# Kernel optimization log

Hardware: AMD Instinct MI355X
Metric: run time of the kernel (lower is better)

Reference implementation:

```python
import jax, jax.numpy as jnp
import numpy as np

ITERS = 10
EPS = 1e-6
TEMPERATURE = 1.0


def setup_inputs() -> dict:
    key = jax.random.key(0)
    S, E = 524288, 64
    logits = jax.random.normal(key, (S, E), dtype=jnp.float32)
    return {"logits": logits, "top_k": 2}


def reference(logits, top_k):
    s, e = logits.shape
    scores = (logits / TEMPERATURE).astype(jnp.float32)
    scores = scores - jnp.max(scores, axis=-1, keepdims=True)
    q = jnp.exp(scores)
    col_target = float(s) / float(max(e, 1))

    def body(q, _):
        q = q / (jnp.sum(q, axis=1, keepdims=True) + EPS)
        q = q / (jnp.sum(q, axis=0, keepdims=True) + EPS) * col_target
        return q, None

    q, _ = jax.lax.scan(body, q, None, length=ITERS)
    q = q / (jnp.sum(q, axis=1, keepdims=True) + EPS)
    vals, idx = jax.lax.top_k(q, top_k)
    w = vals / (jnp.sum(vals, axis=-1, keepdims=True) + EPS)
    return idx.astype(jnp.int64), w.astype(logits.dtype)
```

## Files before the change

kernel.cpp:

```cpp
#include <hip/hip_runtime.h>
#include <math.h>

#define EPS 1e-6f
#define NE 64
#define THREADS 256
#define WPB 4
#define NBLOCKS 1024
#define NWAVES (NBLOCKS * WPB)
#define ITERS 10
#define PF 4

template <int ctrl>
__device__ __forceinline__ float dppf(float x) {
    return __int_as_float(__builtin_amdgcn_update_dpp(
        0, __float_as_int(x), ctrl, 0xf, 0xf, true));
}
template <int ctrl>
__device__ __forceinline__ int dppi(int x) {
    return __builtin_amdgcn_update_dpp(0, x, ctrl, 0xf, 0xf, true);
}

__device__ __forceinline__ float group16_sum(float v) {
    v += dppf<0xB1>(v);
    v += dppf<0x4E>(v);
    v += dppf<0x141>(v);
    v += dppf<0x140>(v);
    return v;
}

#define ARGMAX_STEP(CTRL)                                      \
    {                                                          \
        float ov = dppf<CTRL>(v);                              \
        int oi = dppi<CTRL>(i);                                \
        if (ov > v || (ov == v && oi < i)) { v = ov; i = oi; } \
    }

__device__ __forceinline__ void group16_argmax(float& v, int& i) {
    ARGMAX_STEP(0xB1)
    ARGMAX_STEP(0x4E)
    ARGMAX_STEP(0x141)
    ARGMAX_STEP(0x140)
}

template <bool FIRST>
__global__ __launch_bounds__(THREADS) void sink_pass(
    const float4* __restrict__ logits4, float* __restrict__ r,
    const float* __restrict__ c, float* __restrict__ Pblk, int nquads) {
    const int lane = threadIdx.x & 63;
    const int wib = threadIdx.x >> 6;
    const int g = lane >> 4;
    const int h = lane & 15;
    const int qpw = nquads / NWAVES;
    const int qbase = (blockIdx.x * WPB + wib) * qpw;

    float4 c4;
    if (FIRST) c4 = make_float4(1.f, 1.f, 1.f, 1.f);
    else       c4 = ((const float4*)c)[h];

    const float4* lp = logits4 + (size_t)qbase * 64 + lane;

    float4 buf[PF];
    float rbuf[PF];
#pragma unroll
    for (int p = 0; p < PF; ++p) buf[p] = lp[(size_t)p * 64];
    if (!FIRST) {
#pragma unroll
        for (int p = 0; p < PF; ++p) rbuf[p] = r[(qbase + p) * 4 + g];
    }

    float4 pacc = {0.f, 0.f, 0.f, 0.f};
    const int nb = qpw / PF;
    for (int b = 0; b < nb; ++b) {
        float4 cur[PF];
        float rcur[PF];
#pragma unroll
        for (int p = 0; p < PF; ++p) {
            cur[p] = buf[p];
            if (!FIRST) rcur[p] = rbuf[p];
        }
        if (b + 1 < nb) {
            const float4* np = lp + (size_t)(b + 1) * PF * 64;
#pragma unroll
            for (int p = 0; p < PF; ++p) buf[p] = np[(size_t)p * 64];
            if (!FIRST) {
#pragma unroll
                for (int p = 0; p < PF; ++p)
                    rbuf[p] = r[(qbase + (b + 1) * PF + p) * 4 + g];
            }
        }
#pragma unroll
        for (int p = 0; p < PF; ++p) {
            float4 q;
            q.x = __expf(cur[p].x); q.y = __expf(cur[p].y);
            q.z = __expf(cur[p].z); q.w = __expf(cur[p].w);
            float s = q.x * c4.x + q.y * c4.y + q.z * c4.z + q.w * c4.w;
            s = group16_sum(s);
            float rold = FIRST ? 1.0f : rcur[p];
            float rnew = rold / (rold * s + EPS);
            int row = (qbase + b * PF + p) * 4 + g;
            if (h == 0) r[row] = rnew;
            pacc.x += q.x * rnew; pacc.y += q.y * rnew;
            pacc.z += q.z * rnew; pacc.w += q.w * rnew;
        }
    }

    __shared__ float4 plds[WPB][64];
    plds[wib][lane] = pacc;
    __syncthreads();
    if (threadIdx.x < NE) {
        int j = threadIdx.x;
        int hh = j >> 2, kk = j & 3;
        float t = 0.f;
#pragma unroll
        for (int w = 0; w < WPB; ++w)
#pragma unroll
            for (int gg = 0; gg < 4; ++gg)
                t += ((const float*)&plds[w][gg * 16 + hh])[kk];
        Pblk[blockIdx.x * NE + j] = t;
    }
}

template <bool FIRST>
__global__ __launch_bounds__(1024) void sink_reduce(
    const float* __restrict__ Pblk, float* __restrict__ c, float col_target) {
    const int j = threadIdx.x & 63;
    const int chunk = threadIdx.x >> 6;
    const int per = NBLOCKS / 16;
    float t = 0.f;
    int b0 = chunk * per;
    for (int b = b0; b < b0 + per; ++b) t += Pblk[b * NE + j];
    __shared__ float lds[16][NE];
    lds[chunk][j] = t;
    __syncthreads();
    if (threadIdx.x < NE) {
        float P = 0.f;
#pragma unroll
        for (int k = 0; k < 16; ++k) P += lds[k][threadIdx.x];
        float cj = FIRST ? 1.0f : c[threadIdx.x];
        c[threadIdx.x] = cj * col_target / (cj * P + EPS);
    }
}

__global__ __launch_bounds__(THREADS) void sink_final(
    const float4* __restrict__ logits4, const float* __restrict__ r,
    const float* __restrict__ c, float2* __restrict__ oidx,
    float2* __restrict__ ow, int nquads) {
    const int lane = threadIdx.x & 63;
    const int wib = threadIdx.x >> 6;
    const int g = lane >> 4;
    const int h = lane & 15;
    const int base_col = h * 4;
    const int qpw = nquads / NWAVES;
    const int qbase = (blockIdx.x * WPB + wib) * qpw;

    const float4 c4 = ((const float4*)c)[h];
    const float4* lp = logits4 + (size_t)qbase * 64 + lane;

    float4 buf[PF];
    float rbuf[PF];
#pragma unroll
    for (int p = 0; p < PF; ++p) buf[p] = lp[(size_t)p * 64];
#pragma unroll
    for (int p = 0; p < PF; ++p) rbuf[p] = r[(qbase + p) * 4 + g];

    const int nb = qpw / PF;
    for (int b = 0; b < nb; ++b) {
        float4 cur[PF];
        float rcur[PF];
#pragma unroll
        for (int p = 0; p < PF; ++p) { cur[p] = buf[p]; rcur[p] = rbuf[p]; }
        if (b + 1 < nb) {
            const float4* np = lp + (size_t)(b + 1) * PF * 64;
#pragma unroll
            for (int p = 0; p < PF; ++p) buf[p] = np[(size_t)p * 64];
#pragma unroll
            for (int p = 0; p < PF; ++p)
                rbuf[p] = r[(qbase + (b + 1) * PF + p) * 4 + g];
        }
#pragma unroll
        for (int p = 0; p < PF; ++p) {
            float4 u;
            u.x = __expf(cur[p].x) * c4.x; u.y = __expf(cur[p].y) * c4.y;
            u.z = __expf(cur[p].z) * c4.z; u.w = __expf(cur[p].w) * c4.w;
            float s = group16_sum(u.x + u.y + u.z + u.w);
            float rold = rcur[p];
            float rnew = rold / (rold * s + EPS);
            float4 val;
            val.x = u.x * rnew; val.y = u.y * rnew;
            val.z = u.z * rnew; val.w = u.w * rnew;

            float v = val.x; int i = base_col;
            if (val.y > v) { v = val.y; i = base_col + 1; }
            if (val.z > v) { v = val.z; i = base_col + 2; }
            if (val.w > v) { v = val.w; i = base_col + 3; }
            group16_argmax(v, i);
            float v1 = v; int i1 = i;

            float4 mv;
            mv.x = (i1 == base_col)     ? -INFINITY : val.x;
            mv.y = (i1 == base_col + 1) ? -INFINITY : val.y;
            mv.z = (i1 == base_col + 2) ? -INFINITY : val.z;
            mv.w = (i1 == base_col + 3) ? -INFINITY : val.w;
            v = mv.x; i = base_col;
            if (mv.y > v) { v = mv.y; i = base_col + 1; }
            if (mv.z > v) { v = mv.z; i = base_col + 2; }
            if (mv.w > v) { v = mv.w; i = base_col + 3; }
            group16_argmax(v, i);
            float v2 = v; int i2 = i;

            if (h == 0) {
                int row = (qbase + b * PF + p) * 4 + g;
                float wsum = v1 + v2 + EPS;
                oidx[row] = make_float2((float)i1, (float)i2);
                ow[row] = make_float2(v1 / wsum, v2 / wsum);
            }
        }
    }
}

extern "C" void kernel_launch(void* const* d_in, const int* in_sizes, int n_in,
                              void* d_out, int out_size, void* d_ws, size_t ws_size,
                              hipStream_t stream) {
    const float* logits = (const float*)d_in[0];
    const int S = in_sizes[0] / NE;
    const int nquads = S / 4;
    const float col_target = (float)S / (float)NE;

    float* r = (float*)d_ws;
    float* c = r + S;
    float* Pblk = c + NE;

    float* out = (float*)d_out;
    float2* oidx = (float2*)out;
    float2* ow = (float2*)(out + (size_t)2 * S);

    const float4* l4 = (const float4*)logits;

    sink_pass<true><<<NBLOCKS, THREADS, 0, stream>>>(l4, r, c, Pblk, nquads);
    sink_reduce<true><<<1, 1024, 0, stream>>>(Pblk, c, col_target);
    for (int it = 1; it < ITERS; ++it) {
        sink_pass<false><<<NBLOCKS, THREADS, 0, stream>>>(l4, r, c, Pblk, nquads);
        sink_reduce<false><<<1, 1024, 0, stream>>>(Pblk, c, col_target);
    }
    sink_final<<<NBLOCKS, THREADS, 0, stream>>>(l4, r, c, oidx, ow, nquads);
}
```

Before: 614.0 us.

## Fuse column reduction into pass kernel via last-block atomic counter

Removes the separate single-block sink_reduce launch after each pass. The last block to finish, found through an atomic counter, now reduces the per-block column partials and updates c. Blocks grow from 256 to 1024 threads and drop from 1024 to 256, which shrinks the partial array. This saves ten launches and their serialization gaps, at the cost of a memset, threadfences, and fewer, larger blocks that may lower occupancy or latency hiding.

```diff
diff --git a/kernel.cpp b/kernel.cpp
--- a/kernel.cpp
+++ b/kernel.cpp
@@ -3,10 +3,10 @@
 
 #define EPS 1e-6f
 #define NE 64
-#define THREADS 256
-#define WPB 4
-#define NBLOCKS 1024
-#define NWAVES (NBLOCKS * WPB)
+#define TPB 1024
+#define WPB 16
+#define NBLK 256
+#define NWAVES (NBLK * WPB)
 #define ITERS 10
 #define PF 4
 
@@ -43,11 +43,13 @@
 }
 
 template <bool FIRST>
-__global__ __launch_bounds__(THREADS) void sink_pass(
+__global__ __launch_bounds__(TPB) void sink_pass(
     const float4* __restrict__ logits4, float* __restrict__ r,
-    const float* __restrict__ c, float* __restrict__ Pblk, int nquads) {
-    const int lane = threadIdx.x & 63;
-    const int wib = threadIdx.x >> 6;
+    float* __restrict__ c, float* __restrict__ Pblk,
+    unsigned* __restrict__ counters, int nquads, float col_target, int it) {
+    const int tid = threadIdx.x;
+    const int lane = tid & 63;
+    const int wib = tid >> 6;
     const int g = lane >> 4;
     const int h = lane & 15;
     const int qpw = nquads / NWAVES;
@@ -105,11 +107,11 @@
     }
 
     __shared__ float4 plds[WPB][64];
+    __shared__ int lastflag;
     plds[wib][lane] = pacc;
     __syncthreads();
-    if (threadIdx.x < NE) {
-        int j = threadIdx.x;
-        int hh = j >> 2, kk = j & 3;
+    if (tid < NE) {
+        int j = tid, hh = j >> 2, kk = j & 3;
         float t = 0.f;
 #pragma unroll
         for (int w = 0; w < WPB; ++w)
@@ -117,36 +119,44 @@
             for (int gg = 0; gg < 4; ++gg)
                 t += ((const float*)&plds[w][gg * 16 + hh])[kk];
         Pblk[blockIdx.x * NE + j] = t;
-    }
-}
-
-template <bool FIRST>
-__global__ __launch_bounds__(1024) void sink_reduce(
-    const float* __restrict__ Pblk, float* __restrict__ c, float col_target) {
-    const int j = threadIdx.x & 63;
-    const int chunk = threadIdx.x >> 6;
-    const int per = NBLOCKS / 16;
-    float t = 0.f;
-    int b0 = chunk * per;
-    for (int b = b0; b < b0 + per; ++b) t += Pblk[b * NE + j];
-    __shared__ float lds[16][NE];
-    lds[chunk][j] = t;
+        __threadfence();
+    }
     __syncthreads();
-    if (threadIdx.x < NE) {
-        float P = 0.f;
-#pragma unroll
-        for (int k = 0; k < 16; ++k) P += lds[k][threadIdx.x];
-        float cj = FIRST ? 1.0f : c[threadIdx.x];
-        c[threadIdx.x] = cj * col_target / (cj * P + EPS);
-    }
-}
-
-__global__ __launch_bounds__(THREADS) void sink_final(
+    if (tid == 0) {
+        unsigned old = atomicAdd(&counters[it], 1u);
+        lastflag = (old == (unsigned)(NBLK - 1));
+    }
+    __syncthreads();
+
+    if (lastflag) {
+        __threadfence();
+        float* s_red = (float*)plds;
+        const int j = tid & 63;
+        const int chunk = tid >> 6;
+        float t = 0.f;
+        int b0 = chunk * (NBLK / 16);
+        for (int b = b0; b < b0 + NBLK / 16; ++b) t += Pblk[b * NE + j];
+        __syncthreads();
+        s_red[chunk * NE + j] = t;
+        __syncthreads();
+        if (tid < NE) {
+            float P = 0.f;
+#pragma unroll
+            for (int k = 0; k < 16; ++k) P += s_red[k * NE + tid];
+            float cj = FIRST ? 1.0f : c[tid];
+            c[tid] = cj * col_target / (cj * P + EPS);
+            __threadfence();
+        }
+    }
+}
+
+__global__ __launch_bounds__(TPB) void sink_final(
     const float4* __restrict__ logits4, const float* __restrict__ r,
     const float* __restrict__ c, float2* __restrict__ oidx,
     float2* __restrict__ ow, int nquads) {
-    const int lane = threadIdx.x & 63;
-    const int wib = threadIdx.x >> 6;
+    const int tid = threadIdx.x;
+    const int lane = tid & 63;
+    const int wib = tid >> 6;
     const int g = lane >> 4;
     const int h = lane & 15;
     const int base_col = h * 4;
@@ -229,6 +239,7 @@
     float* r = (float*)d_ws;
     float* c = r + S;
     float* Pblk = c + NE;
+    unsigned* counters = (unsigned*)(Pblk + NBLK * NE);
 
     float* out = (float*)d_out;
     float2* oidx = (float2*)out;
@@ -236,11 +247,11 @@
 
     const float4* l4 = (const float4*)logits;
 
-    sink_pass<true><<<NBLOCKS, THREADS, 0, stream>>>(l4, r, c, Pblk, nquads);
-    sink_reduce<true><<<1, 1024, 0, stream>>>(Pblk, c, col_target);
-    for (int it = 1; it < ITERS; ++it) {
-        sink_pass<false><<<NBLOCKS, THREADS, 0, stream>>>(l4, r, c, Pblk, nquads);
-        sink_reduce<false><<<1, 1024, 0, stream>>>(Pblk, c, col_target);
-    }
-    sink_final<<<NBLOCKS, THREADS, 0, stream>>>(l4, r, c, oidx, ow, nquads);
-}
+    hipMemsetAsync(counters, 0, ITERS * sizeof(unsigned), stream);
+    sink_pass<true><<<NBLK, TPB, 0, stream>>>(l4, r, c, Pblk, counters,
+                                              nquads, col_target, 0);
+    for (int it = 1; it < ITERS; ++it)
+        sink_pass<false><<<NBLK, TPB, 0, stream>>>(l4, r, c, Pblk, counters,
+                                                   nquads, col_target, it);
+    sink_final<<<NBLK, TPB, 0, stream>>>(l4, r, c, oidx, ow, nquads);
+}
```

New measurement: 554.6 us. 1.11x faster.
